# Performance work log

Hardware: AMD Instinct MI355X
Metric: run time of the kernel (lower is better)

## Reference

```python
import jax, jax.numpy as jnp
import numpy as np

EMBED_DIM = 1024
NUM_HEADS = 16
HEAD_DIM = EMBED_DIM // NUM_HEADS
B, N = 8, 1024


def setup_inputs() -> dict:
    key = jax.random.key(0)
    k1, k2, k3, k4, k5, k6 = jax.random.split(key, 6)
    scale = 1.0 / np.sqrt(EMBED_DIM)
    return {
        "x": jax.random.normal(k1, (B, N, EMBED_DIM), dtype=jnp.float32),
        "attn_mask": jax.random.normal(k2, (N, N), dtype=jnp.float32) * 0.1,
        "in_proj_weight": jax.random.normal(k3, (3 * EMBED_DIM, EMBED_DIM), dtype=jnp.float32) * scale,
        "in_proj_bias": jax.random.normal(k4, (3 * EMBED_DIM,), dtype=jnp.float32) * 0.02,
        "out_w": jax.random.normal(k5, (EMBED_DIM, EMBED_DIM), dtype=jnp.float32) * scale,
        "out_b": jax.random.normal(k6, (EMBED_DIM,), dtype=jnp.float32) * 0.02,
    }


def reference(x, attn_mask, in_proj_weight, in_proj_bias, out_w, out_b):
    # x: (B, N, C); fused QKV projection as in forward_direct
    Bn, Nn, C = x.shape
    H, D = NUM_HEADS, HEAD_DIM
    qkv = x @ in_proj_weight.T + in_proj_bias            # (B, N, 3C)
    qkv = qkv.reshape(Bn, Nn, 3, H, D).transpose(2, 0, 3, 1, 4)  # (3, B, H, N, D)
    q, k, v = qkv[0], qkv[1], qkv[2]
    q = q / jnp.sqrt(jnp.asarray(D, dtype=q.dtype))
    attn = jnp.einsum("bhnd,bhmd->bhnm", q, k)           # (B, H, N, N) scores
    attn = attn + attn_mask                              # broadcast over (B, H)
    attn = jax.nn.softmax(attn, axis=-1)
    out = jnp.einsum("bhnm,bhmd->bhnd", attn, v)         # (B, H, N, D)
    out = out.transpose(0, 2, 1, 3).reshape(Bn, Nn, C)   # (B, N, C)
    return out @ out_w.T + out_b
```

## Files before the change

### kernel.cpp

```cpp
#include <hip/hip_runtime.h>


typedef __bf16 bf16x8 __attribute__((ext_vector_type(8)));
typedef float f32x4 __attribute__((ext_vector_type(4)));
typedef unsigned short us4v __attribute__((ext_vector_type(4)));

#define MFMA16 __builtin_amdgcn_mfma_f32_16x16x32_bf16

__device__ __forceinline__ unsigned short f2bf(float f) {
    return __builtin_bit_cast(unsigned short, (__bf16)f);
}

__device__ __forceinline__ us4v cvt4(float4 v) {
    us4v r;
    r.x = f2bf(v.x); r.y = f2bf(v.y); r.z = f2bf(v.z); r.w = f2bf(v.w);
    return r;
}

__device__ __forceinline__ void gl16(const unsigned short* g, unsigned short* l) {
    __builtin_amdgcn_global_load_lds(
        (const __attribute__((address_space(1))) unsigned*)g,
        (__attribute__((address_space(3))) unsigned*)l, 16, 0, 0);
}

__global__ __launch_bounds__(256)
void cvt_bf16(const float* __restrict__ src, unsigned short* __restrict__ dst,
              int n4) {
    const int i = blockIdx.x * 256 + threadIdx.x;
    if (i < n4) {
        float4 v = ((const float4*)src)[i];
        ((us4v*)dst)[i] = cvt4(v);
    }
}

__global__ __launch_bounds__(256, 3)
void qkv_gemm(const unsigned short* __restrict__ xb,
              const unsigned short* __restrict__ wb,
              const float* __restrict__ bias,
              unsigned short* __restrict__ qb, unsigned short* __restrict__ kb,
              unsigned short* __restrict__ vbT)
{
    __shared__ unsigned short lsa[128 * 32];
    __shared__ unsigned short lsb[128 * 32];
    const int tid  = threadIdx.x;
    const int wave = tid >> 6, lane = tid & 63;
    const int quad = lane >> 4, l15 = lane & 15;
    const int rch = (quad ^ ((l15 >> 1) & 3)) * 8;
    const int m0 = blockIdx.x * 128, n0 = blockIdx.y * 128;
    const int wm = (wave & 1) * 64, wn = (wave >> 1) * 64;

    const int srow = wave * 32 + (lane >> 2);
    const int scol = ((lane & 3) ^ ((lane >> 3) & 3)) * 8;
    const unsigned short* ga = xb + (size_t)(m0 + srow) * 1024 + scol;
    const unsigned short* gb = wb + (size_t)(n0 + srow) * 1024 + scol;
    unsigned short* la0 = &lsa[(wave * 32) * 32];
    unsigned short* la1 = &lsa[(wave * 32 + 16) * 32];
    unsigned short* lb0 = &lsb[(wave * 32) * 32];
    unsigned short* lb1 = &lsb[(wave * 32 + 16) * 32];

    f32x4 acc[4][4];
#pragma unroll
    for (int i = 0; i < 4; ++i)
#pragma unroll
        for (int j = 0; j < 4; ++j) acc[i][j] = (f32x4){0.f, 0.f, 0.f, 0.f};

    for (int kt = 0; kt < 32; ++kt) {
        const int k0 = kt * 32;
        __syncthreads();
        gl16(ga + k0, la0);
        gl16(ga + 16 * 1024 + k0, la1);
        gl16(gb + k0, lb0);
        gl16(gb + 16 * 1024 + k0, lb1);
        __syncthreads();
        bf16x8 af[4], bfr[4];
#pragma unroll
        for (int i = 0; i < 4; ++i)
            af[i] = *(const bf16x8*)&lsa[(wm + i * 16 + l15) * 32 + rch];
#pragma unroll
        for (int j = 0; j < 4; ++j)
            bfr[j] = *(const bf16x8*)&lsb[(wn + j * 16 + l15) * 32 + rch];
#pragma unroll
        for (int i = 0; i < 4; ++i)
#pragma unroll
            for (int j = 0; j < 4; ++j)
                acc[i][j] = MFMA16(af[i], bfr[j], acc[i][j], 0, 0, 0);
    }

    const int which = n0 >> 10;
    if (which == 2) {
#pragma unroll
        for (int j = 0; j < 4; ++j) {
            const int n = n0 + wn + j * 16 + l15;
            const int c = n & 1023;
            const int h = c >> 6, d = c & 63;
            const float bv = bias[n];
#pragma unroll
            for (int i = 0; i < 4; ++i) {
                const int m = m0 + wm + i * 16 + quad * 4;
                const int b = m >> 10, s = m & 1023;
                us4v pk;
#pragma unroll
                for (int r = 0; r < 4; ++r) pk[r] = f2bf(acc[i][j][r] + bv);
                *(us4v*)&vbT[(size_t)((b * 16 + h) * 64 + d) * 1024 + s] = pk;
            }
        }
    } else {
        unsigned short* __restrict__ dst = (which == 0) ? qb : kb;
        const float sc = (which == 0) ? 0.125f : 1.0f;
#pragma unroll
        for (int j = 0; j < 4; ++j) {
            const int n = n0 + wn + j * 16 + l15;
            const int c = n & 1023;
            const int h = c >> 6, d = c & 63;
            const float bv = bias[n];
#pragma unroll
            for (int i = 0; i < 4; ++i)
#pragma unroll
                for (int r = 0; r < 4; ++r) {
                    const int m = m0 + wm + i * 16 + quad * 4 + r;
                    const int b = m >> 10, s = m & 1023;
                    const float v = (acc[i][j][r] + bv) * sc;
                    dst[(size_t)((b * 16 + h) * 1024 + s) * 64 + d] = f2bf(v);
                }
        }
    }
}

__global__ __launch_bounds__(256, 4)
void attn_kernel(const unsigned short* __restrict__ qb,
                 const unsigned short* __restrict__ kb,
                 const unsigned short* __restrict__ vbT,
                 const float* __restrict__ mask,
                 unsigned short* __restrict__ ob)
{
    __shared__ unsigned short lsk0[64 * 32];
    __shared__ unsigned short lsk1[64 * 32];
    __shared__ unsigned short lsv0[64 * 32];
    __shared__ unsigned short lsv1[64 * 32];
    __shared__ unsigned short lsp[4][16 * 72];
    const int tid  = threadIdx.x;
    const int wave = tid >> 6, lane = tid & 63;
    const int quad = lane >> 4, l15 = lane & 15;
    const int rch = (quad ^ ((l15 >> 1) & 3)) * 8;
    const int bh = blockIdx.x >> 4;
    const int q0 = (blockIdx.x & 15) * 64;
    const int b = bh >> 4, h = bh & 15;

    const unsigned short* __restrict__ kbase = kb + (size_t)bh * 65536;
    const unsigned short* __restrict__ vtb  = vbT + (size_t)bh * 65536;

    const int scol = ((lane & 3) ^ ((lane >> 3) & 3)) * 8;
    const unsigned short* gk = kbase + (size_t)(wave * 16 + (lane >> 2)) * 64
                                     + scol;
    const unsigned short* gv = vtb + (size_t)(wave * 16 + (lane >> 2)) * 1024
                                   + scol;
    unsigned short* lk0 = &lsk0[(wave * 16) * 32];
    unsigned short* lk1 = &lsk1[(wave * 16) * 32];
    unsigned short* lv0 = &lsv0[(wave * 16) * 32];
    unsigned short* lv1 = &lsv1[(wave * 16) * 32];

    bf16x8 bq0, bq1;
    {
        const unsigned short* qrow =
            qb + (size_t)(bh * 1024 + q0 + wave * 16 + l15) * 64;
        bq0 = *(const bf16x8*)(qrow + quad * 8);
        bq1 = *(const bf16x8*)(qrow + 32 + quad * 8);
    }

    float lsum = 0.f;
    f32x4 oacc[4];
#pragma unroll
    for (int nt = 0; nt < 4; ++nt) oacc[nt] = (f32x4){0.f, 0.f, 0.f, 0.f};

    const float* __restrict__ mrow =
        mask + (size_t)(q0 + wave * 16 + l15) * 1024;
    unsigned short* lp = lsp[wave];

    for (int kt = 0; kt < 16; ++kt) {
        __syncthreads();
        gl16(gk + (size_t)kt * 4096, lk0);
        gl16(gk + (size_t)kt * 4096 + 32, lk1);
        gl16(gv + (size_t)kt * 64, lv0);
        gl16(gv + (size_t)kt * 64 + 32, lv1);
        __syncthreads();

        f32x4 s[4];
#pragma unroll
        for (int nt = 0; nt < 4; ++nt) s[nt] = (f32x4){0.f, 0.f, 0.f, 0.f};
#pragma unroll
        for (int nt = 0; nt < 4; ++nt) {
            s[nt] = MFMA16(*(const bf16x8*)&lsk0[(nt * 16 + l15) * 32 + rch],
                           bq0, s[nt], 0, 0, 0);
            s[nt] = MFMA16(*(const bf16x8*)&lsk1[(nt * 16 + l15) * 32 + rch],
                           bq1, s[nt], 0, 0, 0);
        }

#pragma unroll
        for (int nt = 0; nt < 4; ++nt) {
            const float4 mv =
                *(const float4*)&mrow[kt * 64 + nt * 16 + quad * 4];
            us4v pk;
#pragma unroll
            for (int r = 0; r < 4; ++r) {
                const float p = __expf(s[nt][r] + ((const float*)&mv)[r]);
                lsum += p;
                pk[r] = f2bf(p);
            }
            *(us4v*)&lp[l15 * 72 + nt * 16 + quad * 4] = pk;
        }
        const bf16x8 pb0 = *(const bf16x8*)&lp[l15 * 72 + quad * 8];
        const bf16x8 pb1 = *(const bf16x8*)&lp[l15 * 72 + 32 + quad * 8];

#pragma unroll
        for (int nt = 0; nt < 4; ++nt) {
            oacc[nt] = MFMA16(*(const bf16x8*)&lsv0[(nt * 16 + l15) * 32 + rch],
                              pb0, oacc[nt], 0, 0, 0);
            oacc[nt] = MFMA16(*(const bf16x8*)&lsv1[(nt * 16 + l15) * 32 + rch],
                              pb1, oacc[nt], 0, 0, 0);
        }
    }

    lsum += __shfl_xor(lsum, 16, 64);
    lsum += __shfl_xor(lsum, 32, 64);
    const float inv = 1.0f / lsum;

    unsigned short* orow =
        ob + (size_t)(b * 1024 + q0 + wave * 16 + l15) * 1024 + h * 64;
#pragma unroll
    for (int nt = 0; nt < 4; ++nt) {
        us4v o;
#pragma unroll
        for (int r = 0; r < 4; ++r) o[r] = f2bf(oacc[nt][r] * inv);
        *(us4v*)&orow[nt * 16 + quad * 4] = o;
    }
}

__global__ __launch_bounds__(256, 3)
void out_gemm(const unsigned short* __restrict__ a,
              const unsigned short* __restrict__ wb,
              const float* __restrict__ bias, float* __restrict__ out)
{
    __shared__ unsigned short lsa[128 * 32];
    __shared__ unsigned short lsb[128 * 32];
    const int tid  = threadIdx.x;
    const int wave = tid >> 6, lane = tid & 63;
    const int quad = lane >> 4, l15 = lane & 15;
    const int rch = (quad ^ ((l15 >> 1) & 3)) * 8;
    const int m0 = blockIdx.x * 128, n0 = blockIdx.y * 128;
    const int wm = (wave & 1) * 64, wn = (wave >> 1) * 64;

    const int srow = wave * 32 + (lane >> 2);
    const int scol = ((lane & 3) ^ ((lane >> 3) & 3)) * 8;
    const unsigned short* ga = a + (size_t)(m0 + srow) * 1024 + scol;
    const unsigned short* gb = wb + (size_t)(n0 + srow) * 1024 + scol;
    unsigned short* la0 = &lsa[(wave * 32) * 32];
    unsigned short* la1 = &lsa[(wave * 32 + 16) * 32];
    unsigned short* lb0 = &lsb[(wave * 32) * 32];
    unsigned short* lb1 = &lsb[(wave * 32 + 16) * 32];

    f32x4 acc[4][4];
#pragma unroll
    for (int i = 0; i < 4; ++i)
#pragma unroll
        for (int j = 0; j < 4; ++j) acc[i][j] = (f32x4){0.f, 0.f, 0.f, 0.f};

    for (int kt = 0; kt < 32; ++kt) {
        const int k0 = kt * 32;
        __syncthreads();
        gl16(ga + k0, la0);
        gl16(ga + 16 * 1024 + k0, la1);
        gl16(gb + k0, lb0);
        gl16(gb + 16 * 1024 + k0, lb1);
        __syncthreads();
        bf16x8 af[4], bfr[4];
#pragma unroll
        for (int i = 0; i < 4; ++i)
            af[i] = *(const bf16x8*)&lsa[(wm + i * 16 + l15) * 32 + rch];
#pragma unroll
        for (int j = 0; j < 4; ++j)
            bfr[j] = *(const bf16x8*)&lsb[(wn + j * 16 + l15) * 32 + rch];
#pragma unroll
        for (int i = 0; i < 4; ++i)
#pragma unroll
            for (int j = 0; j < 4; ++j)
                acc[i][j] = MFMA16(af[i], bfr[j], acc[i][j], 0, 0, 0);
    }

#pragma unroll
    for (int j = 0; j < 4; ++j) {
        const int n = n0 + wn + j * 16 + l15;
        const float bv = bias[n];
#pragma unroll
        for (int i = 0; i < 4; ++i)
#pragma unroll
            for (int r = 0; r < 4; ++r) {
                const int m = m0 + wm + i * 16 + quad * 4 + r;
                out[(size_t)m * 1024 + n] = acc[i][j][r] + bv;
            }
    }
}

extern "C" void kernel_launch(void* const* d_in, const int* in_sizes, int n_in,
                              void* d_out, int out_size, void* d_ws, size_t ws_size,
                              hipStream_t stream) {
    const float* x    = (const float*)d_in[0];
    const float* mask = (const float*)d_in[1];
    const float* win  = (const float*)d_in[2];
    const float* bin  = (const float*)d_in[3];
    const float* wout = (const float*)d_in[4];
    const float* bout = (const float*)d_in[5];
    float* out = (float*)d_out;

    char* ws = (char*)d_ws;
    unsigned short* xb = (unsigned short*)(ws);
    unsigned short* ob = (unsigned short*)(ws);
    unsigned short* qb = (unsigned short*)(ws + (size_t)(16 << 20));
    unsigned short* kb = (unsigned short*)(ws + (size_t)(32 << 20));
    unsigned short* vbT = (unsigned short*)(ws + (size_t)(48 << 20));
    unsigned short* winb  = (unsigned short*)d_out;
    unsigned short* woutb = (unsigned short*)((char*)d_out + (size_t)(6 << 20));

    cvt_bf16<<<dim3(8192), 256, 0, stream>>>(x, xb, 8 * 1024 * 1024 / 4);
    cvt_bf16<<<dim3(3072), 256, 0, stream>>>(win, winb, 3 * 1024 * 1024 / 4);
    cvt_bf16<<<dim3(1024), 256, 0, stream>>>(wout, woutb, 1024 * 1024 / 4);
    qkv_gemm<<<dim3(64, 24), 256, 0, stream>>>(xb, winb, bin, qb, kb, vbT);
    attn_kernel<<<dim3(2048), 256, 0, stream>>>(qb, kb, vbT, mask, ob);
    out_gemm<<<dim3(64, 8), 256, 0, stream>>>(ob, woutb, bout, out);
}
```

Before: 292.1 us.

## Double-buffer LDS tiles in GEMMs and attention, load V directly to registers

Adds LDS double buffering to the QKV and output GEMMs and to the K tiles in attention. The next tile is prefetched with global_load_lds while the current one is computed, which cuts one barrier per iteration. In attention, V fragments are read straight from global memory into registers instead of through LDS. Block indices are remapped so neighbouring blocks spread across (b,h), and s_setprio raises priority around the MFMA sections. The cost is twice the LDS per GEMM block, which may lower occupancy. Attention also issues uncoalesced-ish global V loads every iteration, and the barrier placement relies on global_load_lds completing before the trailing sync.

Result: slower. 376.3 us (+28.8%).

```diff
diff --git a/kernel.cpp b/kernel.cpp
--- a/kernel.cpp
+++ b/kernel.cpp
@@ -40,8 +40,8 @@
               unsigned short* __restrict__ qb, unsigned short* __restrict__ kb,
               unsigned short* __restrict__ vbT)
 {
-    __shared__ unsigned short lsa[128 * 32];
-    __shared__ unsigned short lsb[128 * 32];
+    __shared__ unsigned short lsa[2][128 * 32];
+    __shared__ unsigned short lsb[2][128 * 32];
     const int tid  = threadIdx.x;
     const int wave = tid >> 6, lane = tid & 63;
     const int quad = lane >> 4, l15 = lane & 15;
@@ -53,10 +53,8 @@
     const int scol = ((lane & 3) ^ ((lane >> 3) & 3)) * 8;
     const unsigned short* ga = xb + (size_t)(m0 + srow) * 1024 + scol;
     const unsigned short* gb = wb + (size_t)(n0 + srow) * 1024 + scol;
-    unsigned short* la0 = &lsa[(wave * 32) * 32];
-    unsigned short* la1 = &lsa[(wave * 32 + 16) * 32];
-    unsigned short* lb0 = &lsb[(wave * 32) * 32];
-    unsigned short* lb1 = &lsb[(wave * 32 + 16) * 32];
+    const int so0 = (wave * 32) * 32;
+    const int so1 = (wave * 32 + 16) * 32;
 
     f32x4 acc[4][4];
 #pragma unroll
@@ -64,26 +62,37 @@
 #pragma unroll
         for (int j = 0; j < 4; ++j) acc[i][j] = (f32x4){0.f, 0.f, 0.f, 0.f};
 
+    gl16(ga, &lsa[0][so0]);
+    gl16(ga + 16 * 1024, &lsa[0][so1]);
+    gl16(gb, &lsb[0][so0]);
+    gl16(gb + 16 * 1024, &lsb[0][so1]);
+    __syncthreads();
+
+    int buf = 0;
     for (int kt = 0; kt < 32; ++kt) {
-        const int k0 = kt * 32;
-        __syncthreads();
-        gl16(ga + k0, la0);
-        gl16(ga + 16 * 1024 + k0, la1);
-        gl16(gb + k0, lb0);
-        gl16(gb + 16 * 1024 + k0, lb1);
-        __syncthreads();
+        if (kt < 31) {
+            const int k0 = (kt + 1) * 32;
+            gl16(ga + k0, &lsa[buf ^ 1][so0]);
+            gl16(ga + 16 * 1024 + k0, &lsa[buf ^ 1][so1]);
+            gl16(gb + k0, &lsb[buf ^ 1][so0]);
+            gl16(gb + 16 * 1024 + k0, &lsb[buf ^ 1][so1]);
+        }
+        const unsigned short* pa = lsa[buf];
+        const unsigned short* pb = lsb[buf];
         bf16x8 af[4], bfr[4];
 #pragma unroll
         for (int i = 0; i < 4; ++i)
-            af[i] = *(const bf16x8*)&lsa[(wm + i * 16 + l15) * 32 + rch];
+            af[i] = *(const bf16x8*)&pa[(wm + i * 16 + l15) * 32 + rch];
 #pragma unroll
         for (int j = 0; j < 4; ++j)
-            bfr[j] = *(const bf16x8*)&lsb[(wn + j * 16 + l15) * 32 + rch];
+            bfr[j] = *(const bf16x8*)&pb[(wn + j * 16 + l15) * 32 + rch];
 #pragma unroll
         for (int i = 0; i < 4; ++i)
 #pragma unroll
             for (int j = 0; j < 4; ++j)
                 acc[i][j] = MFMA16(af[i], bfr[j], acc[i][j], 0, 0, 0);
+        __syncthreads();
+        buf ^= 1;
     }
 
     const int which = n0 >> 10;
@@ -133,17 +142,16 @@
                  const float* __restrict__ mask,
                  unsigned short* __restrict__ ob)
 {
-    __shared__ unsigned short lsk0[64 * 32];
-    __shared__ unsigned short lsk1[64 * 32];
-    __shared__ unsigned short lsv0[64 * 32];
-    __shared__ unsigned short lsv1[64 * 32];
+    __shared__ unsigned short lsk[2][2][64 * 32];
     __shared__ unsigned short lsp[4][16 * 72];
     const int tid  = threadIdx.x;
     const int wave = tid >> 6, lane = tid & 63;
     const int quad = lane >> 4, l15 = lane & 15;
     const int rch = (quad ^ ((l15 >> 1) & 3)) * 8;
-    const int bh = blockIdx.x >> 4;
-    const int q0 = (blockIdx.x & 15) * 64;
+    const int p  = blockIdx.x;
+    const int lg = (p & 7) * 256 + (p >> 3);
+    const int bh = lg >> 4;
+    const int q0 = (lg & 15) * 64;
     const int b = bh >> 4, h = bh & 15;
 
     const unsigned short* __restrict__ kbase = kb + (size_t)bh * 65536;
@@ -152,12 +160,9 @@
     const int scol = ((lane & 3) ^ ((lane >> 3) & 3)) * 8;
     const unsigned short* gk = kbase + (size_t)(wave * 16 + (lane >> 2)) * 64
                                      + scol;
-    const unsigned short* gv = vtb + (size_t)(wave * 16 + (lane >> 2)) * 1024
-                                   + scol;
-    unsigned short* lk0 = &lsk0[(wave * 16) * 32];
-    unsigned short* lk1 = &lsk1[(wave * 16) * 32];
-    unsigned short* lv0 = &lsv0[(wave * 16) * 32];
-    unsigned short* lv1 = &lsv1[(wave * 16) * 32];
+    const int so = (wave * 16) * 32;
+
+    const unsigned short* gvf = vtb + (size_t)l15 * 1024 + quad * 8;
 
     bf16x8 bq0, bq1;
     {
@@ -176,24 +181,37 @@
         mask + (size_t)(q0 + wave * 16 + l15) * 1024;
     unsigned short* lp = lsp[wave];
 
+    gl16(gk, &lsk[0][0][so]);
+    gl16(gk + 32, &lsk[0][1][so]);
+    __syncthreads();
+
+    int buf = 0;
     for (int kt = 0; kt < 16; ++kt) {
-        __syncthreads();
-        gl16(gk + (size_t)kt * 4096, lk0);
-        gl16(gk + (size_t)kt * 4096 + 32, lk1);
-        gl16(gv + (size_t)kt * 64, lv0);
-        gl16(gv + (size_t)kt * 64 + 32, lv1);
-        __syncthreads();
-
+        if (kt < 15) {
+            gl16(gk + (size_t)(kt + 1) * 4096, &lsk[buf ^ 1][0][so]);
+            gl16(gk + (size_t)(kt + 1) * 4096 + 32, &lsk[buf ^ 1][1][so]);
+        }
+        bf16x8 vf0[4], vf1[4];
+#pragma unroll
+        for (int nt = 0; nt < 4; ++nt) {
+            vf0[nt] = *(const bf16x8*)(gvf + (size_t)nt * 16 * 1024 + kt * 64);
+            vf1[nt] = *(const bf16x8*)(gvf + (size_t)nt * 16 * 1024 + kt * 64 + 32);
+        }
+
+        const unsigned short* rk0 = lsk[buf][0];
+        const unsigned short* rk1 = lsk[buf][1];
         f32x4 s[4];
 #pragma unroll
         for (int nt = 0; nt < 4; ++nt) s[nt] = (f32x4){0.f, 0.f, 0.f, 0.f};
+        __builtin_amdgcn_s_setprio(1);
 #pragma unroll
         for (int nt = 0; nt < 4; ++nt) {
-            s[nt] = MFMA16(*(const bf16x8*)&lsk0[(nt * 16 + l15) * 32 + rch],
+            s[nt] = MFMA16(*(const bf16x8*)&rk0[(nt * 16 + l15) * 32 + rch],
                            bq0, s[nt], 0, 0, 0);
-            s[nt] = MFMA16(*(const bf16x8*)&lsk1[(nt * 16 + l15) * 32 + rch],
+            s[nt] = MFMA16(*(const bf16x8*)&rk1[(nt * 16 + l15) * 32 + rch],
                            bq1, s[nt], 0, 0, 0);
         }
+        __builtin_amdgcn_s_setprio(0);
 
 #pragma unroll
         for (int nt = 0; nt < 4; ++nt) {
@@ -202,22 +220,25 @@
             us4v pk;
 #pragma unroll
             for (int r = 0; r < 4; ++r) {
-                const float p = __expf(s[nt][r] + ((const float*)&mv)[r]);
-                lsum += p;
-                pk[r] = f2bf(p);
+                const float pe = __expf(s[nt][r] + ((const float*)&mv)[r]);
+                lsum += pe;
+                pk[r] = f2bf(pe);
             }
             *(us4v*)&lp[l15 * 72 + nt * 16 + quad * 4] = pk;
         }
         const bf16x8 pb0 = *(const bf16x8*)&lp[l15 * 72 + quad * 8];
         const bf16x8 pb1 = *(const bf16x8*)&lp[l15 * 72 + 32 + quad * 8];
 
+        __builtin_amdgcn_s_setprio(1);
 #pragma unroll
         for (int nt = 0; nt < 4; ++nt) {
-            oacc[nt] = MFMA16(*(const bf16x8*)&lsv0[(nt * 16 + l15) * 32 + rch],
-                              pb0, oacc[nt], 0, 0, 0);
-            oacc[nt] = MFMA16(*(const bf16x8*)&lsv1[(nt * 16 + l15) * 32 + rch],
-                              pb1, oacc[nt], 0, 0, 0);
-        }
+            oacc[nt] = MFMA16(vf0[nt], pb0, oacc[nt], 0, 0, 0);
+            oacc[nt] = MFMA16(vf1[nt], pb1, oacc[nt], 0, 0, 0);
+        }
+        __builtin_amdgcn_s_setprio(0);
+
+        __syncthreads();
+        buf ^= 1;
     }
 
     lsum += __shfl_xor(lsum, 16, 64);
@@ -240,8 +261,8 @@
               const unsigned short* __restrict__ wb,
               const float* __restrict__ bias, float* __restrict__ out)
 {
-    __shared__ unsigned short lsa[128 * 32];
-    __shared__ unsigned short lsb[128 * 32];
+    __shared__ unsigned short lsa[2][128 * 32];
+    __shared__ unsigned short lsb[2][128 * 32];
     const int tid  = threadIdx.x;
     const int wave = tid >> 6, lane = tid & 63;
     const int quad = lane >> 4, l15 = lane & 15;
@@ -253,10 +274,8 @@
     const int scol = ((lane & 3) ^ ((lane >> 3) & 3)) * 8;
     const unsigned short* ga = a + (size_t)(m0 + srow) * 1024 + scol;
     const unsigned short* gb = wb + (size_t)(n0 + srow) * 1024 + scol;
-    unsigned short* la0 = &lsa[(wave * 32) * 32];
-    unsigned short* la1 = &lsa[(wave * 32 + 16) * 32];
-    unsigned short* lb0 = &lsb[(wave * 32) * 32];
-    unsigned short* lb1 = &lsb[(wave * 32 + 16) * 32];
+    const int so0 = (wave * 32) * 32;
+    const int so1 = (wave * 32 + 16) * 32;
 
     f32x4 acc[4][4];
 #pragma unroll
@@ -264,26 +283,37 @@
 #pragma unroll
         for (int j = 0; j < 4; ++j) acc[i][j] = (f32x4){0.f, 0.f, 0.f, 0.f};
 
+    gl16(ga, &lsa[0][so0]);
+    gl16(ga + 16 * 1024, &lsa[0][so1]);
+    gl16(gb, &lsb[0][so0]);
+    gl16(gb + 16 * 1024, &lsb[0][so1]);
+    __syncthreads();
+
+    int buf = 0;
     for (int kt = 0; kt < 32; ++kt) {
-        const int k0 = kt * 32;
-        __syncthreads();
-        gl16(ga + k0, la0);
-        gl16(ga + 16 * 1024 + k0, la1);
-        gl16(gb + k0, lb0);
-        gl16(gb + 16 * 1024 + k0, lb1);
-        __syncthreads();
+        if (kt < 31) {
+            const int k0 = (kt + 1) * 32;
+            gl16(ga + k0, &lsa[buf ^ 1][so0]);
+            gl16(ga + 16 * 1024 + k0, &lsa[buf ^ 1][so1]);
+            gl16(gb + k0, &lsb[buf ^ 1][so0]);
+            gl16(gb + 16 * 1024 + k0, &lsb[buf ^ 1][so1]);
+        }
+        const unsigned short* pa = lsa[buf];
+        const unsigned short* pb = lsb[buf];
         bf16x8 af[4], bfr[4];
 #pragma unroll
         for (int i = 0; i < 4; ++i)
-            af[i] = *(const bf16x8*)&lsa[(wm + i * 16 + l15) * 32 + rch];
+            af[i] = *(const bf16x8*)&pa[(wm + i * 16 + l15) * 32 + rch];
 #pragma unroll
         for (int j = 0; j < 4; ++j)
-            bfr[j] = *(const bf16x8*)&lsb[(wn + j * 16 + l15) * 32 + rch];
+            bfr[j] = *(const bf16x8*)&pb[(wn + j * 16 + l15) * 32 + rch];
 #pragma unroll
         for (int i = 0; i < 4; ++i)
 #pragma unroll
             for (int j = 0; j < 4; ++j)
                 acc[i][j] = MFMA16(af[i], bfr[j], acc[i][j], 0, 0, 0);
+        __syncthreads();
+        buf ^= 1;
     }
 
 #pragma unroll
```
